# Kernel tuning notes

Hardware: AMD Instinct MI355X
Metric: run time of the kernel (lower is better)

Reference implementation:

```python
import jax, jax.numpy as jnp
import numpy as np

EPS_LN = 1e-5
EPS_COS = 1e-8
EPS_AREA = 5e-4


def _ln(x, g, b):
    m = jnp.mean(x, axis=-1, keepdims=True)
    v = jnp.mean((x - m) ** 2, axis=-1, keepdims=True)
    return (x - m) / jnp.sqrt(v + EPS_LN) * g + b


def _wgap(f, m):
    # f: (b, N, c), m: (b, N) -> (b, c); matches masked avg_pool2d trick
    num = jnp.einsum('bnc,bn->bc', f, m)
    den = jnp.sum(m, axis=1, keepdims=True) + EPS_AREA
    return num / den


def _cos_tok(k, p):
    # k: (b, N, c) tokens vs p: (b, c) prototype, cosine over channel dim
    dot = jnp.einsum('bnc,bc->bn', k, p)
    nk = jnp.linalg.norm(k, axis=-1)
    np_ = jnp.linalg.norm(p, axis=-1, keepdims=True)
    return dot / (jnp.maximum(nk, EPS_COS) * jnp.maximum(np_, EPS_COS))


def _cos_vec(a, b):
    # a, b: (b, c) -> (b,)
    dot = jnp.sum(a * b, axis=-1)
    na = jnp.linalg.norm(a, axis=-1)
    nb = jnp.linalg.norm(b, axis=-1)
    return dot / (jnp.maximum(na, EPS_COS) * jnp.maximum(nb, EPS_COS))


def _mlp(x, W1, b1, W2, b2):
    h = jax.nn.gelu(x @ W1.T + b1, approximate=False)
    return h @ W2.T + b2


def setup_inputs() -> dict:
    key = jax.random.key(0)
    ks = jax.random.split(key, 32)
    b, H, W, c = 8, 64, 64, 512
    N = H * W
    hid = 4 * c
    s = 0.02
    inp = {
        'x': jax.random.normal(ks[0], (b, N, c), jnp.float32),
        'y': jax.random.normal(ks[1], (b, N, c), jnp.float32),
        'mask': (jax.random.uniform(ks[2], (b, N)) > 0.5).astype(jnp.float32),
        'pro_pred': jax.random.uniform(ks[3], (b, 1, H, W), jnp.float32),
        'g1': jnp.ones((c,), jnp.float32), 'beta1': jnp.zeros((c,), jnp.float32),
        'g2': jnp.ones((c,), jnp.float32), 'beta2': jnp.zeros((c,), jnp.float32),
        'Wq': jax.random.normal(ks[4], (c, c)) * s,
        'Wk': jax.random.normal(ks[5], (c, c)) * s,
        'Wv': jax.random.normal(ks[6], (c, c)) * s,
        'Wx1': jax.random.normal(ks[7], (c, 2 * c)) * s,
        'Wx2': jax.random.normal(ks[8], (c, 2 * c)) * s,
        'Wfx': jax.random.normal(ks[9], (c, 2 * c)) * s,
        'Wy1': jax.random.normal(ks[10], (c, 2 * c)) * s,
        'Wy2': jax.random.normal(ks[11], (c, 2 * c)) * s,
        'Wfy': jax.random.normal(ks[12], (c, 2 * c)) * s,
        'W1x': jax.random.normal(ks[13], (hid, c)) * s, 'b1x': jnp.zeros((hid,)),
        'W2x': jax.random.normal(ks[14], (c, hid)) * s, 'b2x': jnp.zeros((c,)),
        'W1y': jax.random.normal(ks[15], (hid, c)) * s, 'b1y': jnp.zeros((hid,)),
        'W2y': jax.random.normal(ks[16], (c, hid)) * s, 'b2y': jnp.zeros((c,)),
        'h': 64, 'w': 64,
    }
    return inp


def reference(x, y, mask, pro_pred, g1, beta1, g2, beta2, Wq, Wk, Wv,
              Wx1, Wx2, Wfx, Wy1, Wy2, Wfy,
              W1x, b1x, W2x, b2x, W1y, b1y, W2y, b2y, h, w):
    b, N, c = x.shape
    x_skip, y_skip = x, y
    xn = _ln(x, g1, beta1)
    yn = _ln(y, g1, beta1)
    q = yn @ Wq.T            # support features (b, N, c)
    k = xn @ Wk.T            # query features
    v = xn @ Wv.T

    m = mask                 # (b, N)
    fg_pro = _wgap(q, m)             # (b, c)
    bg_pro = _wgap(q, 1.0 - m)

    sim_fg = _cos_tok(k, fg_pro) * 10.0   # (b, N)
    sim_bg = _cos_tok(k, bg_pro) * 10.0
    logits = jnp.stack([sim_bg, sim_fg], axis=1)     # (b, 2, N)
    pseudo = jax.nn.softmax(logits, axis=1)

    query_fg1 = _wgap(v, pseudo[:, 1, :])            # (b, c)
    s1 = (_cos_vec(query_fg1, fg_pro)[:, None] + 1.0) / 2.0
    pro1 = s1 * fg_pro + (1.0 - s1) * query_fg1      # (b, c)

    query_fg2 = _wgap(v, pro_pred.reshape(b, N))
    s2 = (_cos_vec(query_fg2, fg_pro)[:, None] + 1.0) / 2.0
    pro2 = s2 * fg_pro + (1.0 - s2) * query_fg2

    p1 = jnp.broadcast_to(pro1[:, None, :], (b, N, c))
    p2 = jnp.broadcast_to(pro2[:, None, :], (b, N, c))

    x1 = jnp.concatenate([x_skip, p1], axis=-1) @ Wx1.T
    x2 = jnp.concatenate([x_skip, p2], axis=-1) @ Wx2.T
    x_merge = jnp.concatenate([x1, x2], axis=-1) @ Wfx.T + x_skip

    y1 = jnp.concatenate([y_skip, p1], axis=-1) @ Wy1.T
    y2 = jnp.concatenate([y_skip, p2], axis=-1) @ Wy2.T
    y_merge = jnp.concatenate([y1, y2], axis=-1) @ Wfy.T + y_skip

    x_out = x + _mlp(_ln(x_merge, g2, beta2), W1x, b1x, W2x, b2x)
    y_out = y + _mlp(_ln(y_merge, g2, beta2), W1y, b1y, W2y, b2y)
    pseudo_mask = pseudo.reshape(b, 2, h, w)
    return x_out, y_out, pseudo_mask
```

## Files before the change

kernel.cpp:

```cpp
#include <hip/hip_runtime.h>
#include <stdint.h>

typedef unsigned short u16;
typedef unsigned int   u32;

typedef __attribute__((ext_vector_type(8))) __bf16 bf16x8;
typedef __attribute__((ext_vector_type(4))) float  f32x4;

#define GLD_LDS(g, l) __builtin_amdgcn_global_load_lds( \
    (__attribute__((address_space(1))) void*)(g),        \
    (__attribute__((address_space(3))) void*)(l), 16, 0, 0)

__device__ __forceinline__ float bf2f(u16 h) {
    union { u32 u; float f; } c; c.u = ((u32)h) << 16; return c.f;
}
__device__ __forceinline__ u16 f2bf(float f) {
    union { float f; u32 u; } c; c.f = f;
    return (u16)((c.u + 0x7FFFu + ((c.u >> 16) & 1u)) >> 16);
}
__device__ __forceinline__ u32 pack2(float a, float b) {
    return (u32)f2bf(a) | ((u32)f2bf(b) << 16);
}
__device__ __forceinline__ uint4 pack8(float4 a, float4 b) {
    return make_uint4(pack2(a.x, a.y), pack2(a.z, a.w), pack2(b.x, b.y), pack2(b.z, b.w));
}
__device__ __forceinline__ void unpack8(uint4 u, float v[8]) {
    v[0] = bf2f((u16)(u.x & 0xffff)); v[1] = bf2f((u16)(u.x >> 16));
    v[2] = bf2f((u16)(u.y & 0xffff)); v[3] = bf2f((u16)(u.y >> 16));
    v[4] = bf2f((u16)(u.z & 0xffff)); v[5] = bf2f((u16)(u.z >> 16));
    v[6] = bf2f((u16)(u.w & 0xffff)); v[7] = bf2f((u16)(u.w >> 16));
}
__device__ __forceinline__ float wsum(float v) {
#pragma unroll
    for (int o = 32; o > 0; o >>= 1) v += __shfl_xor(v, o, 64);
    return v;
}
__device__ __forceinline__ float fast_gelu(float x) {
    const float u = x * (1.f + 0.044715f * x * x);
    return x / (1.f + __expf(-1.5957691216f * u));
}

__global__ __launch_bounds__(256)
void cvt_kernel(const float* __restrict__ in, u16* __restrict__ out, int n8)
{
    const int i = blockIdx.x * 256 + threadIdx.x;
    if (i < n8) {
        const float* p = in + (size_t)i * 8;
        float4 a = *(const float4*)p, b = *(const float4*)(p + 4);
        *(uint4*)(out + (size_t)i * 8) = pack8(a, b);
    }
}

template<bool IN16, bool RAW>
__global__ __launch_bounds__(256)
void ln_kernel(const void* __restrict__ in, u16* __restrict__ out,
               const float* __restrict__ g, const float* __restrict__ be,
               u16* __restrict__ raw_out)
{
    const int lane = threadIdx.x & 63;
    const size_t row = (size_t)blockIdx.x * 4 + (threadIdx.x >> 6);
    const size_t base = row * 512 + lane * 8;
    float v[8];
    if constexpr (IN16) {
        unpack8(*(const uint4*)((const u16*)in + base), v);
    } else {
        const float* p = (const float*)in + base;
        float4 a = *(const float4*)p, b = *(const float4*)(p + 4);
        v[0]=a.x; v[1]=a.y; v[2]=a.z; v[3]=a.w; v[4]=b.x; v[5]=b.y; v[6]=b.z; v[7]=b.w;
    }
    if constexpr (RAW) {
        u32 ro[4];
#pragma unroll
        for (int i = 0; i < 4; ++i) ro[i] = pack2(v[2*i], v[2*i+1]);
        *(uint4*)(raw_out + base) = make_uint4(ro[0], ro[1], ro[2], ro[3]);
    }
    float s = 0.f, ss = 0.f;
#pragma unroll
    for (int i = 0; i < 8; ++i) { s += v[i]; ss += v[i] * v[i]; }
    s = wsum(s); ss = wsum(ss);
    const float mean = s * (1.f / 512.f);
    const float rstd = rsqrtf(ss * (1.f / 512.f) - mean * mean + 1e-5f);
    const float* gp = g + lane * 8;
    const float* bp = be + lane * 8;
    u32 o[4];
#pragma unroll
    for (int i = 0; i < 4; ++i) {
        u16 lo = f2bf((v[2*i]   - mean) * rstd * gp[2*i]   + bp[2*i]);
        u16 hi = f2bf((v[2*i+1] - mean) * rstd * gp[2*i+1] + bp[2*i+1]);
        o[i] = (u32)lo | ((u32)hi << 16);
    }
    *(uint4*)(out + base) = make_uint4(o[0], o[1], o[2], o[3]);
}

template<bool IS16>
__device__ __forceinline__ void load_pair(const void* P, size_t off, size_t rstep,
                                          uint4& r0, uint4& r1)
{
    if constexpr (IS16) {
        const u16* p = (const u16*)P + off;
        r0 = *(const uint4*)p;
        r1 = *(const uint4*)(p + rstep);
    } else {
        const float* p = (const float*)P + off;
        float4 a0 = *(const float4*)p,           a1 = *(const float4*)(p + 4);
        float4 b0 = *(const float4*)(p + rstep), b1 = *(const float4*)(p + rstep + 4);
        r0 = pack8(a0, a1);
        r1 = pack8(b0, b1);
    }
}

template<int EPI, bool OUT16>
__global__ __launch_bounds__(512)
void gemm3_kernel(const u16* __restrict__ A, const u16* __restrict__ B,
                  void* __restrict__ Cp, int N, int K,
                  const float* __restrict__ bias_b,
                  const float* __restrict__ bias_v,
                  const float* __restrict__ skip)
{
    __shared__ u16 sA[2][128 * 32];
    __shared__ u16 sB[2][256 * 32];
    const int t = threadIdx.x;
    const int w = t >> 6;
    const int lane = t & 63;
    const int lr = lane & 15;
    const int lk = lane >> 4;
    const int bm0 = blockIdx.x * 128;
    const int bn0 = blockIdx.y * 256;
    const int wrow = (w >> 2) * 64;
    const int wcol = (w & 3) * 64;

    f32x4 acc[4][4];
#pragma unroll
    for (int m = 0; m < 4; ++m)
#pragma unroll
        for (int n = 0; n < 4; ++n) acc[m][n] = (f32x4){0.f, 0.f, 0.f, 0.f};

    const int scol = ((t & 3) ^ ((t >> 3) & 3)) * 8;
    const u16* gA = A + (size_t)(bm0 + (t >> 2)) * K + scol;
    const u16* gB = B + (size_t)(bn0 + (t >> 2)) * K + scol;
    const size_t rstep = (size_t)128 * K;
    const int wo = w << 9;
    const int sa = (lk ^ ((lr >> 1) & 3)) * 8;

    GLD_LDS(gA, sA[0] + wo);
    GLD_LDS(gB, sB[0] + wo);
    GLD_LDS(gB + rstep, sB[0] + 4096 + wo);
    __syncthreads();

    int cur = 0;
    for (int kt = 32; kt <= K; kt += 32) {
        if (kt < K) {
            const int nxt = cur ^ 1;
            GLD_LDS(gA + kt, sA[nxt] + wo);
            GLD_LDS(gB + kt, sB[nxt] + wo);
            GLD_LDS(gB + kt + rstep, sB[nxt] + 4096 + wo);
        }
        bf16x8 af[4], bfr[4];
#pragma unroll
        for (int m = 0; m < 4; ++m)
            af[m] = *(const bf16x8*)&sA[cur][(wrow + m * 16 + lr) * 32 + sa];
#pragma unroll
        for (int n = 0; n < 4; ++n)
            bfr[n] = *(const bf16x8*)&sB[cur][(wcol + n * 16 + lr) * 32 + sa];
#pragma unroll
        for (int m = 0; m < 4; ++m)
#pragma unroll
            for (int n = 0; n < 4; ++n)
                acc[m][n] = __builtin_amdgcn_mfma_f32_16x16x32_bf16(af[m], bfr[n], acc[m][n], 0, 0, 0);
        if (kt < K) { __syncthreads(); cur ^= 1; }
    }

#pragma unroll
    for (int m = 0; m < 4; ++m) {
#pragma unroll
        for (int n = 0; n < 4; ++n) {
            const int col = bn0 + wcol + n * 16 + lr;
#pragma unroll
            for (int r = 0; r < 4; ++r) {
                const int row = bm0 + wrow + m * 16 + lk * 4 + r;
                const size_t idx = (size_t)row * N + col;
                float vv = acc[m][n][r];
                if (EPI == 1) vv += bias_b[(size_t)(row >> 12) * N + col] + skip[idx];
                if (EPI == 2) { vv += bias_v[col]; vv = fast_gelu(vv); }
                if (EPI == 3) vv += bias_v[col] + skip[idx];
                if (OUT16) ((u16*)Cp)[idx] = f2bf(vv);
                else       ((float*)Cp)[idx] = vv;
            }
        }
    }
}

template<int EPI, bool OUT16>
__global__ __launch_bounds__(256)
void gemm2_kernel(const u16* __restrict__ A, const u16* __restrict__ B,
                  void* __restrict__ Cp, int N, int K,
                  const float* __restrict__ bias_b,
                  const float* __restrict__ bias_v,
                  const float* __restrict__ skip)
{
    __shared__ u16 sA[2][128 * 32];
    __shared__ u16 sB[2][128 * 32];
    const int t = threadIdx.x;
    const int w = t >> 6;
    const int lane = t & 63;
    const int lr = lane & 15;
    const int lk = lane >> 4;
    const int bm0 = blockIdx.x * 128;
    const int bn0 = blockIdx.y * 128;
    const int wrow = (w >> 1) * 64;
    const int wcol = (w & 1) * 64;

    f32x4 acc[4][4];
#pragma unroll
    for (int m = 0; m < 4; ++m)
#pragma unroll
        for (int n = 0; n < 4; ++n) acc[m][n] = (f32x4){0.f, 0.f, 0.f, 0.f};

    const int scol = ((t & 3) ^ ((t >> 3) & 3)) * 8;
    const u16* gA = A + (size_t)(bm0 + (t >> 2)) * K + scol;
    const u16* gB = B + (size_t)(bn0 + (t >> 2)) * K + scol;
    const size_t rstep = (size_t)64 * K;
    const int wo = w << 9;
    const int sa = (lk ^ ((lr >> 1) & 3)) * 8;

    GLD_LDS(gA, sA[0] + wo); GLD_LDS(gA + rstep, sA[0] + wo + 2048);
    GLD_LDS(gB, sB[0] + wo); GLD_LDS(gB + rstep, sB[0] + wo + 2048);
    __syncthreads();

    int cur = 0;
    for (int kt = 32; kt <= K; kt += 32) {
        if (kt < K) {
            const int nxt = cur ^ 1;
            GLD_LDS(gA + kt, sA[nxt] + wo); GLD_LDS(gA + kt + rstep, sA[nxt] + wo + 2048);
            GLD_LDS(gB + kt, sB[nxt] + wo); GLD_LDS(gB + kt + rstep, sB[nxt] + wo + 2048);
        }
        bf16x8 af[4], bfr[4];
#pragma unroll
        for (int m = 0; m < 4; ++m)
            af[m] = *(const bf16x8*)&sA[cur][(wrow + m * 16 + lr) * 32 + sa];
#pragma unroll
        for (int n = 0; n < 4; ++n)
            bfr[n] = *(const bf16x8*)&sB[cur][(wcol + n * 16 + lr) * 32 + sa];
#pragma unroll
        for (int m = 0; m < 4; ++m)
#pragma unroll
            for (int n = 0; n < 4; ++n)
                acc[m][n] = __builtin_amdgcn_mfma_f32_16x16x32_bf16(af[m], bfr[n], acc[m][n], 0, 0, 0);
        if (kt < K) { __syncthreads(); cur ^= 1; }
    }

#pragma unroll
    for (int m = 0; m < 4; ++m) {
#pragma unroll
        for (int n = 0; n < 4; ++n) {
            const int col = bn0 + wcol + n * 16 + lr;
#pragma unroll
            for (int r = 0; r < 4; ++r) {
                const int row = bm0 + wrow + m * 16 + lk * 4 + r;
                const size_t idx = (size_t)row * N + col;
                float vv = acc[m][n][r];
                if (EPI == 1) vv += bias_b[(size_t)(row >> 12) * N + col] + skip[idx];
                if (EPI == 2) { vv += bias_v[col]; vv = fast_gelu(vv); }
                if (EPI == 3) vv += bias_v[col] + skip[idx];
                if (OUT16) ((u16*)Cp)[idx] = f2bf(vv);
                else       ((float*)Cp)[idx] = vv;
            }
        }
    }
}

template<int WM>
__global__ __launch_bounds__(512)
void gemm3_red_kernel(const u16* __restrict__ A, const u16* __restrict__ B, int K,
                      const float* __restrict__ wa, const float* __restrict__ wb,
                      float* __restrict__ acc1, float* __restrict__ acc2)
{
    __shared__ u16 sA[2][128 * 32];
    __shared__ u16 sB[2][256 * 32];
    __shared__ float sred[8][2][64];
    const int t = threadIdx.x;
    const int w = t >> 6;
    const int lane = t & 63;
    const int lr = lane & 15;
    const int lk = lane >> 4;
    const int bm0 = blockIdx.x * 128;
    const int bn0 = blockIdx.y * 256;
    const int wrow = (w >> 2) * 64;
    const int wcol = (w & 3) * 64;

    f32x4 acc[4][4];
#pragma unroll
    for (int m = 0; m < 4; ++m)
#pragma unroll
        for (int n = 0; n < 4; ++n) acc[m][n] = (f32x4){0.f, 0.f, 0.f, 0.f};

    const int scol = ((t & 3) ^ ((t >> 3) & 3)) * 8;
    const u16* gA = A + (size_t)(bm0 + (t >> 2)) * K + scol;
    const u16* gB = B + (size_t)(bn0 + (t >> 2)) * K + scol;
    const size_t rstep = (size_t)128 * K;
    const int wo = w << 9;
    const int sa = (lk ^ ((lr >> 1) & 3)) * 8;

    GLD_LDS(gA, sA[0] + wo);
    GLD_LDS(gB, sB[0] + wo);
    GLD_LDS(gB + rstep, sB[0] + 4096 + wo);
    __syncthreads();

    int cur = 0;
    for (int kt = 32; kt <= K; kt += 32) {
        if (kt < K) {
            const int nxt = cur ^ 1;
            GLD_LDS(gA + kt, sA[nxt] + wo);
            GLD_LDS(gB + kt, sB[nxt] + wo);
            GLD_LDS(gB + kt + rstep, sB[nxt] + 4096 + wo);
        }
        bf16x8 af[4], bfr[4];
#pragma unroll
        for (int m = 0; m < 4; ++m)
            af[m] = *(const bf16x8*)&sA[cur][(wrow + m * 16 + lr) * 32 + sa];
#pragma unroll
        for (int n = 0; n < 4; ++n)
            bfr[n] = *(const bf16x8*)&sB[cur][(wcol + n * 16 + lr) * 32 + sa];
#pragma unroll
        for (int m = 0; m < 4; ++m)
#pragma unroll
            for (int n = 0; n < 4; ++n)
                acc[m][n] = __builtin_amdgcn_mfma_f32_16x16x32_bf16(af[m], bfr[n], acc[m][n], 0, 0, 0);
        if (kt < K) { __syncthreads(); cur ^= 1; }
    }

    float w1v[16], w2v[16];
#pragma unroll
    for (int m = 0; m < 4; ++m)
#pragma unroll
        for (int r = 0; r < 4; ++r) {
            const int row = bm0 + wrow + m * 16 + lk * 4 + r;
            if (WM == 0) { float mm = wa[row]; w1v[m*4+r] = mm; w2v[m*4+r] = 1.f - mm; }
            else         { w1v[m*4+r] = wa[row]; w2v[m*4+r] = wb[row]; }
        }
    __syncthreads();
#pragma unroll
    for (int n = 0; n < 4; ++n) {
        float s1 = 0.f, s2 = 0.f;
#pragma unroll
        for (int m = 0; m < 4; ++m)
#pragma unroll
            for (int r = 0; r < 4; ++r) {
                s1 += acc[m][n][r] * w1v[m*4+r];
                s2 += acc[m][n][r] * w2v[m*4+r];
            }
        s1 += __shfl_xor(s1, 16, 64); s1 += __shfl_xor(s1, 32, 64);
        s2 += __shfl_xor(s2, 16, 64); s2 += __shfl_xor(s2, 32, 64);
        if (lk == 0) { sred[w][0][n*16+lr] = s1; sred[w][1][n*16+lr] = s2; }
    }
    __syncthreads();
    if (t < 256) {
        const int strip = t >> 6, c = t & 63;
        const float v1 = sred[strip][0][c] + sred[strip + 4][0][c];
        const float v2 = sred[strip][1][c] + sred[strip + 4][1][c];
        const int col = bn0 + strip * 64 + c;
        const int b = bm0 >> 12;
        atomicAdd(&acc1[b * 512 + col], v1);
        atomicAdd(&acc2[b * 512 + col], v2);
    }
}

template<int EPI, bool A16, bool B16, bool OUT16>
__global__ __launch_bounds__(256)
void gemm_kernel(const void* __restrict__ Ap, const void* __restrict__ Wp,
                 void* __restrict__ Cp, int N, int K,
                 const float* __restrict__ bias_b,
                 const float* __restrict__ bias_v,
                 const float* __restrict__ skip)
{
    __shared__ u16 sA[128 * 32];
    __shared__ u16 sB[128 * 32];
    const int t = threadIdx.x;
    const int w = t >> 6;
    const int lane = t & 63;
    const int lr = lane & 15;
    const int lk = lane >> 4;
    const int bm0 = blockIdx.x * 128;
    const int bn0 = blockIdx.y * 128;
    const int wrow = (w >> 1) * 64;
    const int wcol = (w & 1) * 64;

    f32x4 acc[4][4];
#pragma unroll
    for (int m = 0; m < 4; ++m)
#pragma unroll
        for (int n = 0; n < 4; ++n) acc[m][n] = (f32x4){0.f, 0.f, 0.f, 0.f};

    const size_t aoff = (size_t)(bm0 + (t >> 2)) * K + (t & 3) * 8;
    const size_t boff = (size_t)(bn0 + (t >> 2)) * K + (t & 3) * 8;
    const size_t rstep = (size_t)64 * K;
    u16* dA = sA + 8 * t;
    u16* dB = sB + 8 * t;

    for (int kt = 0; kt < K; kt += 32) {
        uint4 ra0, ra1, rb0, rb1;
        load_pair<A16>(Ap, aoff + kt, rstep, ra0, ra1);
        load_pair<B16>(Wp, boff + kt, rstep, rb0, rb1);
        __syncthreads();
        *(uint4*)dA = ra0; *(uint4*)(dA + 2048) = ra1;
        *(uint4*)dB = rb0; *(uint4*)(dB + 2048) = rb1;
        __syncthreads();
        bf16x8 af[4], bfr[4];
#pragma unroll
        for (int m = 0; m < 4; ++m)
            af[m] = *(const bf16x8*)&sA[(wrow + m * 16 + lr) * 32 + lk * 8];
#pragma unroll
        for (int n = 0; n < 4; ++n)
            bfr[n] = *(const bf16x8*)&sB[(wcol + n * 16 + lr) * 32 + lk * 8];
#pragma unroll
        for (int m = 0; m < 4; ++m)
#pragma unroll
            for (int n = 0; n < 4; ++n)
                acc[m][n] = __builtin_amdgcn_mfma_f32_16x16x32_bf16(af[m], bfr[n], acc[m][n], 0, 0, 0);
    }

#pragma unroll
    for (int m = 0; m < 4; ++m) {
#pragma unroll
        for (int n = 0; n < 4; ++n) {
            const int col = bn0 + wcol + n * 16 + lr;
#pragma unroll
            for (int r = 0; r < 4; ++r) {
                const int row = bm0 + wrow + m * 16 + lk * 4 + r;
                const size_t idx = (size_t)row * N + col;
                float vv = acc[m][n][r];
                if (EPI == 1) vv += bias_b[(size_t)(row >> 12) * N + col] + skip[idx];
                if (EPI == 2) { vv += bias_v[col]; vv = fast_gelu(vv); }
                if (EPI == 3) vv += bias_v[col] + skip[idx];
                if (OUT16) ((u16*)Cp)[idx] = f2bf(vv);
                else       ((float*)Cp)[idx] = vv;
            }
        }
    }
}

template<int WM>
__global__ __launch_bounds__(256)
void gemm_red_kernel(const u16* __restrict__ A, const float* __restrict__ W, int K,
                     const float* __restrict__ wa, const float* __restrict__ wb,
                     float* __restrict__ acc1, float* __restrict__ acc2)
{
    __shared__ u16 sA[128 * 32];
    __shared__ u16 sB[128 * 32];
    __shared__ float sred[4][2][64];
    const int t = threadIdx.x;
    const int w = t >> 6;
    const int lane = t & 63;
    const int lr = lane & 15;
    const int lk = lane >> 4;
    const int bm0 = blockIdx.x * 128;
    const int bn0 = blockIdx.y * 128;
    const int wrow = (w >> 1) * 64;
    const int wcol = (w & 1) * 64;

    f32x4 acc[4][4];
#pragma unroll
    for (int m = 0; m < 4; ++m)
#pragma unroll
        for (int n = 0; n < 4; ++n) acc[m][n] = (f32x4){0.f, 0.f, 0.f, 0.f};

    const size_t aoff = (size_t)(bm0 + (t >> 2)) * K + (t & 3) * 8;
    const size_t boff = (size_t)(bn0 + (t >> 2)) * K + (t & 3) * 8;
    const size_t rstep = (size_t)64 * K;
    u16* dA = sA + 8 * t;
    u16* dB = sB + 8 * t;

    for (int kt = 0; kt < K; kt += 32) {
        uint4 ra0, ra1, rb0, rb1;
        load_pair<true >(A, aoff + kt, rstep, ra0, ra1);
        load_pair<false>(W, boff + kt, rstep, rb0, rb1);
        __syncthreads();
        *(uint4*)dA = ra0; *(uint4*)(dA + 2048) = ra1;
        *(uint4*)dB = rb0; *(uint4*)(dB + 2048) = rb1;
        __syncthreads();
        bf16x8 af[4], bfr[4];
#pragma unroll
        for (int m = 0; m < 4; ++m)
            af[m] = *(const bf16x8*)&sA[(wrow + m * 16 + lr) * 32 + lk * 8];
#pragma unroll
        for (int n = 0; n < 4; ++n)
            bfr[n] = *(const bf16x8*)&sB[(wcol + n * 16 + lr) * 32 + lk * 8];
#pragma unroll
        for (int m = 0; m < 4; ++m)
#pragma unroll
            for (int n = 0; n < 4; ++n)
                acc[m][n] = __builtin_amdgcn_mfma_f32_16x16x32_bf16(af[m], bfr[n], acc[m][n], 0, 0, 0);
    }

    float w1v[16], w2v[16];
#pragma unroll
    for (int m = 0; m < 4; ++m)
#pragma unroll
        for (int r = 0; r < 4; ++r) {
            const int row = bm0 + wrow + m * 16 + lk * 4 + r;
            if (WM == 0) { float mm = wa[row]; w1v[m*4+r] = mm; w2v[m*4+r] = 1.f - mm; }
            else         { w1v[m*4+r] = wa[row]; w2v[m*4+r] = wb[row]; }
        }
#pragma unroll
    for (int n = 0; n < 4; ++n) {
        float s1 = 0.f, s2 = 0.f;
#pragma unroll
        for (int m = 0; m < 4; ++m)
#pragma unroll
            for (int r = 0; r < 4; ++r) {
                s1 += acc[m][n][r] * w1v[m*4+r];
                s2 += acc[m][n][r] * w2v[m*4+r];
            }
        s1 += __shfl_xor(s1, 16, 64); s1 += __shfl_xor(s1, 32, 64);
        s2 += __shfl_xor(s2, 16, 64); s2 += __shfl_xor(s2, 32, 64);
        if (lk == 0) { sred[w][0][n*16+lr] = s1; sred[w][1][n*16+lr] = s2; }
    }
    __syncthreads();
    if (t < 128) {
        const int half = t >> 6, c = t & 63;
        const float v1 = sred[half][0][c] + sred[half + 2][0][c];
        const float v2 = sred[half][1][c] + sred[half + 2][1][c];
        const int col = bn0 + half * 64 + c;
        const int b = bm0 >> 12;
        atomicAdd(&acc1[b * 512 + col], v1);
        atomicAdd(&acc2[b * 512 + col], v2);
    }
}

__global__ __launch_bounds__(256)
void rowsum_kernel(const float* __restrict__ in, float* __restrict__ out)
{
    __shared__ float sred[4];
    const int b = blockIdx.x, t = threadIdx.x;
    float s = 0.f;
    for (int i = 0; i < 16; ++i) s += in[b * 4096 + t + i * 256];
    s = wsum(s);
    if ((t & 63) == 0) sred[t >> 6] = s;
    __syncthreads();
    if (t == 0) out[b] = sred[0] + sred[1] + sred[2] + sred[3];
}

__global__ __launch_bounds__(512)
void proto_fin_kernel(const float* __restrict__ fgacc, const float* __restrict__ bgacc,
                      const float* __restrict__ denfg, float* __restrict__ fg_pro,
                      float* __restrict__ bg_pro, float* __restrict__ nfg, float* __restrict__ nbg)
{
    __shared__ float sred[16];
    const int b = blockIdx.x, c = threadIdx.x;
    const float d = denfg[b];
    const float fg = fgacc[b * 512 + c] / (d + 5e-4f);
    const float bg = bgacc[b * 512 + c] / ((4096.f - d) + 5e-4f);
    fg_pro[b * 512 + c] = fg; bg_pro[b * 512 + c] = bg;
    float s1 = wsum(fg * fg), s2 = wsum(bg * bg);
    if ((c & 63) == 0) { sred[c >> 6] = s1; sred[8 + (c >> 6)] = s2; }
    __syncthreads();
    if (c == 0) {
        float a = 0.f, bb = 0.f;
        for (int i = 0; i < 8; ++i) { a += sred[i]; bb += sred[8 + i]; }
        nfg[b] = sqrtf(a); nbg[b] = sqrtf(bb);
    }
}

__global__ __launch_bounds__(256)
void sim_kernel(const u16* __restrict__ k, const float* __restrict__ fg_pro,
                const float* __restrict__ bg_pro, const float* __restrict__ nfg,
                const float* __restrict__ nbg, float* __restrict__ pseudo_fg,
                float* __restrict__ pm)
{
    const int lane = threadIdx.x & 63;
    const int token = blockIdx.x * 4 + (threadIdx.x >> 6);
    const int b = token >> 12, n = token & 4095;
    uint4 u = *(const uint4*)(k + (size_t)token * 512 + lane * 8);
    float kv[8]; unpack8(u, kv);
    const float* fp = fg_pro + b * 512 + lane * 8;
    const float* bp = bg_pro + b * 512 + lane * 8;
    float dfg = 0.f, dbg = 0.f, kk = 0.f;
#pragma unroll
    for (int i = 0; i < 8; ++i) { dfg += kv[i] * fp[i]; dbg += kv[i] * bp[i]; kk += kv[i] * kv[i]; }
    dfg = wsum(dfg); dbg = wsum(dbg); kk = wsum(kk);
    const float nk = fmaxf(sqrtf(kk), 1e-8f);
    const float sfg = 10.f * dfg / (nk * fmaxf(nfg[b], 1e-8f));
    const float sbg = 10.f * dbg / (nk * fmaxf(nbg[b], 1e-8f));
    const float pfg = 1.f / (1.f + expf(sbg - sfg));
    if (lane == 0) {
        pseudo_fg[token] = pfg;
        pm[(size_t)b * 8192 + 4096 + n] = pfg;
        pm[(size_t)b * 8192 + n] = 1.f - pfg;
    }
}

__global__ __launch_bounds__(512)
void proto2_kernel(const float* __restrict__ q1acc, const float* __restrict__ q2acc,
                   const float* __restrict__ denq1, const float* __restrict__ denq2,
                   const float* __restrict__ fg_pro, const float* __restrict__ nfg,
                   float* __restrict__ pro1, float* __restrict__ pro2)
{
    __shared__ float sred[32];
    __shared__ float s1s, s2s;
    const int b = blockIdx.x, c = threadIdx.x;
    const float q1 = q1acc[b * 512 + c] / (denq1[b] + 5e-4f);
    const float q2 = q2acc[b * 512 + c] / (denq2[b] + 5e-4f);
    const float fg = fg_pro[b * 512 + c];
    float r0 = wsum(q1 * fg), r1 = wsum(q1 * q1), r2 = wsum(q2 * fg), r3 = wsum(q2 * q2);
    const int wv = c >> 6;
    if ((c & 63) == 0) { sred[wv] = r0; sred[8 + wv] = r1; sred[16 + wv] = r2; sred[24 + wv] = r3; }
    __syncthreads();
    if (c == 0) {
        float d1 = 0.f, n1 = 0.f, d2 = 0.f, n2 = 0.f;
        for (int i = 0; i < 8; ++i) { d1 += sred[i]; n1 += sred[8+i]; d2 += sred[16+i]; n2 += sred[24+i]; }
        const float nf = fmaxf(nfg[b], 1e-8f);
        s1s = (d1 / (fmaxf(sqrtf(n1), 1e-8f) * nf) + 1.f) * 0.5f;
        s2s = (d2 / (fmaxf(sqrtf(n2), 1e-8f) * nf) + 1.f) * 0.5f;
    }
    __syncthreads();
    pro1[b * 512 + c] = s1s * fg + (1.f - s1s) * q1;
    pro2[b * 512 + c] = s2s * fg + (1.f - s2s) * q2;
}

__global__ __launch_bounds__(256)
void mmcomb_kernel(const float* __restrict__ Wf, const float* __restrict__ W1,
                   const float* __restrict__ W2, u16* __restrict__ Mout)
{
    const int i = blockIdx.x * 16 + threadIdx.x;
    const int o = blockIdx.y * 16 + threadIdx.y;
    float s = 0.f;
    for (int j = 0; j < 512; ++j) {
        s += Wf[o * 1024 + j]       * W1[j * 1024 + i];
        s += Wf[o * 1024 + 512 + j] * W2[j * 1024 + i];
    }
    Mout[o * 512 + i] = f2bf(s);
}

__global__ __launch_bounds__(512)
void tvec_kernel(const float* __restrict__ W, const float* __restrict__ p, float* __restrict__ tout)
{
    const int lane = threadIdx.x & 63;
    const int j = blockIdx.x * 8 + (threadIdx.x >> 6);
    const int b = blockIdx.y;
    const float* wr = W + (size_t)j * 1024 + 512 + lane * 8;
    const float* pr = p + b * 512 + lane * 8;
    float4 w0 = *(const float4*)wr, w1 = *(const float4*)(wr + 4);
    float4 p0 = *(const float4*)pr, p1 = *(const float4*)(pr + 4);
    float s = w0.x*p0.x + w0.y*p0.y + w0.z*p0.z + w0.w*p0.w
            + w1.x*p1.x + w1.y*p1.y + w1.z*p1.z + w1.w*p1.w;
    s = wsum(s);
    if (lane == 0) tout[b * 512 + j] = s;
}

__global__ __launch_bounds__(512)
void biascomb_kernel(const float* __restrict__ Wf, const float* __restrict__ t1,
                     const float* __restrict__ t2, float* __restrict__ bias)
{
    const int lane = threadIdx.x & 63;
    const int o = blockIdx.x * 8 + (threadIdx.x >> 6);
    const int b = blockIdx.y;
    const float* w1 = Wf + (size_t)o * 1024 + lane * 8;
    const float* tp1 = t1 + b * 512 + lane * 8;
    const float* tp2 = t2 + b * 512 + lane * 8;
    float s = 0.f;
#pragma unroll
    for (int h = 0; h < 2; ++h) {
        const float* wv = w1 + h * 512;
        const float* tp = h ? tp2 : tp1;
        float4 a0 = *(const float4*)wv, a1 = *(const float4*)(wv + 4);
        float4 b0 = *(const float4*)tp, b1 = *(const float4*)(tp + 4);
        s += a0.x*b0.x + a0.y*b0.y + a0.z*b0.z + a0.w*b0.w
           + a1.x*b1.x + a1.y*b1.y + a1.z*b1.z + a1.w*b1.w;
    }
    s = wsum(s);
    if (lane == 0) bias[b * 512 + o] = s;
}

extern "C" void kernel_launch(void* const* d_in, const int* in_sizes, int n_in,
                              void* d_out, int out_size, void* d_ws, size_t ws_size,
                              hipStream_t stream)
{
    const float* x   = (const float*)d_in[0];
    const float* y   = (const float*)d_in[1];
    const float* mask= (const float*)d_in[2];
    const float* pp  = (const float*)d_in[3];
    const float* g1  = (const float*)d_in[4];
    const float* be1 = (const float*)d_in[5];
    const float* g2  = (const float*)d_in[6];
    const float* be2 = (const float*)d_in[7];
    const float* Wq  = (const float*)d_in[8];
    const float* Wk  = (const float*)d_in[9];
    const float* Wv  = (const float*)d_in[10];
    const float* Wx1 = (const float*)d_in[11];
    const float* Wx2 = (const float*)d_in[12];
    const float* Wfx = (const float*)d_in[13];
    const float* Wy1 = (const float*)d_in[14];
    const float* Wy2 = (const float*)d_in[15];
    const float* Wfy = (const float*)d_in[16];
    const float* W1x = (const float*)d_in[17];
    const float* b1x = (const float*)d_in[18];
    const float* W2x = (const float*)d_in[19];
    const float* b2x = (const float*)d_in[20];
    const float* W1y = (const float*)d_in[21];
    const float* b1y = (const float*)d_in[22];
    const float* W2y = (const float*)d_in[23];
    const float* b2y = (const float*)d_in[24];

    if (ws_size < 69206016u) return;
    const bool fast = ws_size >= 78643200u;
    const bool huge = ws_size >= 145752064u;

    float* outx = (float*)d_out;
    float* outy = outx + 16777216;
    float* pmf  = outx + 33554432;

    char* wsb = (char*)d_ws;
    float* fsm = (float*)wsb;
    float* fgacc  = fsm;
    float* bgacc  = fsm + 4096;
    float* q1acc  = fsm + 8192;
    float* q2acc  = fsm + 12288;
    float* denq1  = fsm + 16384;
    float* denfg  = fsm + 16392;
    float* denq2  = fsm + 16400;
    float* nfg    = fsm + 16408;
    float* nbg    = fsm + 16416;
    float* fg_pro = fsm + 16424;
    float* bg_pro = fsm + 20520;
    float* pro1   = fsm + 24616;
    float* pro2   = fsm + 28712;
    float* t1x    = fsm + 32808;
    float* t2x    = fsm + 36904;
    float* t1y    = fsm + 41000;
    float* t2y    = fsm + 45096;
    float* bias_x = fsm + 49192;
    float* bias_y = fsm + 53288;
    float* pseudo = fsm + 57384;

    hipMemsetAsync(fsm, 0, 65568, stream);

    if (fast) {
        u16* Mx   = (u16*)(wsb + 0x60000);
        u16* My   = (u16*)(wsb + 0xE0000);
        u16* Wqb  = (u16*)(wsb + 0x160000);
        u16* Wkb  = (u16*)(wsb + 0x1E0000);
        u16* Wvb  = (u16*)(wsb + 0x260000);
        u16* W1xb = (u16*)(wsb + 0x2E0000);
        u16* W2xb = (u16*)(wsb + 0x4E0000);
        u16* W1yb = (u16*)(wsb + 0x6E0000);
        u16* W2yb = (u16*)(wsb + 0x8E0000);
        u16* WS0  = (u16*)(wsb + 0xB00000);
        u16* WS1  = WS0 + 16777216;
        u16* WS2  = WS1 + 16777216;

        u16* OX0 = (u16*)outx;
        u16* OX1 = OX0 + 16777216;
        u16* OY  = (u16*)outy;

        cvt_kernel<<<128, 256, 0, stream>>>(Wq,  Wqb,  32768);
        cvt_kernel<<<128, 256, 0, stream>>>(Wk,  Wkb,  32768);
        cvt_kernel<<<128, 256, 0, stream>>>(Wv,  Wvb,  32768);
        cvt_kernel<<<512, 256, 0, stream>>>(W1x, W1xb, 131072);
        cvt_kernel<<<512, 256, 0, stream>>>(W2x, W2xb, 131072);
        cvt_kernel<<<512, 256, 0, stream>>>(W1y, W1yb, 131072);
        cvt_kernel<<<512, 256, 0, stream>>>(W2y, W2yb, 131072);
        mmcomb_kernel<<<dim3(32, 32), dim3(16, 16), 0, stream>>>(Wfx, Wx1, Wx2, Mx);
        mmcomb_kernel<<<dim3(32, 32), dim3(16, 16), 0, stream>>>(Wfy, Wy1, Wy2, My);

        ln_kernel<false, true><<<8192, 256, 0, stream>>>(x, WS0, g1, be1, OX0);
        ln_kernel<false, true><<<8192, 256, 0, stream>>>(y, WS1, g1, be1, OY);

        dim3 gq(256, 2);
        gemm3_red_kernel<0><<<gq, 512, 0, stream>>>(WS1, Wqb, 512, mask, nullptr, fgacc, bgacc);
        rowsum_kernel<<<8, 256, 0, stream>>>(mask, denfg);
        rowsum_kernel<<<8, 256, 0, stream>>>(pp, denq2);
        proto_fin_kernel<<<8, 512, 0, stream>>>(fgacc, bgacc, denfg, fg_pro, bg_pro, nfg, nbg);

        gemm3_kernel<0, true><<<gq, 512, 0, stream>>>(WS0, Wkb, OX1, 512, 512, nullptr, nullptr, nullptr);
        sim_kernel<<<8192, 256, 0, stream>>>(OX1, fg_pro, bg_pro, nfg, nbg, pseudo, pmf);
        rowsum_kernel<<<8, 256, 0, stream>>>(pseudo, denq1);

        gemm3_red_kernel<1><<<gq, 512, 0, stream>>>(WS0, Wvb, 512, pseudo, pp, q1acc, q2acc);
        proto2_kernel<<<8, 512, 0, stream>>>(q1acc, q2acc, denq1, denq2, fg_pro, nfg, pro1, pro2);

        dim3 gtv(64, 8);
        tvec_kernel<<<gtv, 512, 0, stream>>>(Wx1, pro1, t1x);
        tvec_kernel<<<gtv, 512, 0, stream>>>(Wx2, pro2, t2x);
        tvec_kernel<<<gtv, 512, 0, stream>>>(Wy1, pro1, t1y);
        tvec_kernel<<<gtv, 512, 0, stream>>>(Wy2, pro2, t2y);
        biascomb_kernel<<<gtv, 512, 0, stream>>>(Wfx, t1x, t2x, bias_x);
        biascomb_kernel<<<gtv, 512, 0, stream>>>(Wfy, t1y, t2y, bias_y);

        gemm3_kernel<1, true><<<gq, 512, 0, stream>>>(OX0, Mx, WS0, 512, 512, bias_x, nullptr, x);
        ln_kernel<true, false><<<8192, 256, 0, stream>>>(WS0, WS1, g2, be2, nullptr);
        gemm3_kernel<1, true><<<gq, 512, 0, stream>>>(OY, My, WS0, 512, 512, bias_y, nullptr, y);
        ln_kernel<true, false><<<8192, 256, 0, stream>>>(WS0, WS0, g2, be2, nullptr);

        for (int ch = 0; ch < 2; ++ch) {
            const size_t ro = (size_t)ch * 16384 * 512;
            gemm3_kernel<2, true><<<dim3(128, 8), 512, 0, stream>>>(WS1 + ro, W1xb, OY, 2048, 512, nullptr, b1x, nullptr);
            gemm2_kernel<3, false><<<dim3(128, 4), 256, 0, stream>>>(OY, W2xb, outx + ro, 512, 2048, nullptr, b2x, x + ro);
        }

        if (huge) {
            for (int ch = 0; ch < 2; ++ch) {
                const size_t ro = (size_t)ch * 16384 * 512;
                gemm3_kernel<2, true><<<dim3(128, 8), 512, 0, stream>>>(WS0 + ro, W1yb, WS2, 2048, 512, nullptr, b1y, nullptr);
                gemm2_kernel<3, false><<<dim3(128, 4), 256, 0, stream>>>(WS2, W2yb, outy + ro, 512, 2048, nullptr, b2y, y + ro);
            }
        } else {
            for (int ch = 0; ch < 4; ++ch) {
                const size_t ro = (size_t)ch * 8192 * 512;
                gemm3_kernel<2, true><<<dim3(64, 8), 512, 0, stream>>>(WS0 + ro, W1yb, WS1, 2048, 512, nullptr, b1y, nullptr);
                gemm2_kernel<3, false><<<dim3(64, 4), 256, 0, stream>>>(WS1, W2yb, outy + ro, 512, 2048, nullptr, b2y, y + ro);
            }
        }
    } else {
        u16* Mx  = (u16*)(wsb + 360608);
        u16* My  = (u16*)(wsb + 884896);
        u16* WS0 = (u16*)(wsb + 2097152);
        u16* WS1 = (u16*)(wsb + 35651584);

        ln_kernel<false, false><<<8192, 256, 0, stream>>>(x, WS0, g1, be1, nullptr);
        ln_kernel<false, false><<<8192, 256, 0, stream>>>(y, WS1, g1, be1, nullptr);

        dim3 g512(256, 4);
        gemm_red_kernel<0><<<g512, 256, 0, stream>>>(WS1, Wq, 512, mask, nullptr, fgacc, bgacc);
        rowsum_kernel<<<8, 256, 0, stream>>>(mask, denfg);
        rowsum_kernel<<<8, 256, 0, stream>>>(pp, denq2);
        proto_fin_kernel<<<8, 512, 0, stream>>>(fgacc, bgacc, denfg, fg_pro, bg_pro, nfg, nbg);

        gemm_kernel<0, true, false, true><<<g512, 256, 0, stream>>>(WS0, Wk, WS1, 512, 512, nullptr, nullptr, nullptr);
        sim_kernel<<<8192, 256, 0, stream>>>(WS1, fg_pro, bg_pro, nfg, nbg, pseudo, pmf);
        rowsum_kernel<<<8, 256, 0, stream>>>(pseudo, denq1);

        gemm_red_kernel<1><<<g512, 256, 0, stream>>>(WS0, Wv, 512, pseudo, pp, q1acc, q2acc);
        proto2_kernel<<<8, 512, 0, stream>>>(q1acc, q2acc, denq1, denq2, fg_pro, nfg, pro1, pro2);

        mmcomb_kernel<<<dim3(32, 32), dim3(16, 16), 0, stream>>>(Wfx, Wx1, Wx2, Mx);
        mmcomb_kernel<<<dim3(32, 32), dim3(16, 16), 0, stream>>>(Wfy, Wy1, Wy2, My);
        dim3 gtv(64, 8);
        tvec_kernel<<<gtv, 512, 0, stream>>>(Wx1, pro1, t1x);
        tvec_kernel<<<gtv, 512, 0, stream>>>(Wx2, pro2, t2x);
        tvec_kernel<<<gtv, 512, 0, stream>>>(Wy1, pro1, t1y);
        tvec_kernel<<<gtv, 512, 0, stream>>>(Wy2, pro2, t2y);
        biascomb_kernel<<<gtv, 512, 0, stream>>>(Wfx, t1x, t2x, bias_x);
        biascomb_kernel<<<gtv, 512, 0, stream>>>(Wfy, t1y, t2y, bias_y);

        gemm_kernel<1, false, true, true><<<g512, 256, 0, stream>>>(x, Mx, WS0, 512, 512, bias_x, nullptr, x);
        ln_kernel<true, false><<<8192, 256, 0, stream>>>(WS0, WS1, g2, be2, nullptr);
        for (int ch = 0; ch < 4; ++ch) {
            const size_t ro = (size_t)ch * 8192 * 512;
            gemm_kernel<2, true, false, true><<<dim3(64, 16), 256, 0, stream>>>(WS1 + ro, W1x, WS0, 2048, 512, nullptr, b1x, nullptr);
            gemm_kernel<3, true, false, false><<<dim3(64, 4), 256, 0, stream>>>(WS0, W2x, outx + ro, 512, 2048, nullptr, b2x, x + ro);
        }
        gemm_kernel<1, false, true, true><<<g512, 256, 0, stream>>>(y, My, WS0, 512, 512, bias_y, nullptr, y);
        ln_kernel<true, false><<<8192, 256, 0, stream>>>(WS0, WS1, g2, be2, nullptr);
        for (int ch = 0; ch < 4; ++ch) {
            const size_t ro = (size_t)ch * 8192 * 512;
            gemm_kernel<2, true, false, true><<<dim3(64, 16), 256, 0, stream>>>(WS1 + ro, W1y, WS0, 2048, 512, nullptr, b1y, nullptr);
            gemm_kernel<3, true, false, false><<<dim3(64, 4), 256, 0, stream>>>(WS0, W2y, outy + ro, 512, 2048, nullptr, b2y, y + ro);
        }
    }
    (void)in_sizes; (void)n_in; (void)out_size;
}
```

Baseline: 903.6 us.

## Enlarge GEMM block tile to 256x256 with K-step 64

```diff
diff --git a/kernel.cpp b/kernel.cpp
--- a/kernel.cpp
+++ b/kernel.cpp
@@ -111,73 +111,82 @@
 
 template<int EPI, bool OUT16>
 __global__ __launch_bounds__(512)
-void gemm3_kernel(const u16* __restrict__ A, const u16* __restrict__ B,
+void gemm5_kernel(const u16* __restrict__ A, const u16* __restrict__ B,
                   void* __restrict__ Cp, int N, int K,
                   const float* __restrict__ bias_b,
                   const float* __restrict__ bias_v,
                   const float* __restrict__ skip)
 {
-    __shared__ u16 sA[2][128 * 32];
-    __shared__ u16 sB[2][256 * 32];
+    __shared__ u16 sA[2][256 * 64];
+    __shared__ u16 sB[2][256 * 64];
     const int t = threadIdx.x;
     const int w = t >> 6;
     const int lane = t & 63;
     const int lr = lane & 15;
     const int lk = lane >> 4;
-    const int bm0 = blockIdx.x * 128;
+    const int bm0 = blockIdx.x * 256;
     const int bn0 = blockIdx.y * 256;
-    const int wrow = (w >> 2) * 64;
-    const int wcol = (w & 3) * 64;
-
-    f32x4 acc[4][4];
-#pragma unroll
-    for (int m = 0; m < 4; ++m)
+    const int wr = (w >> 2) * 128;
+    const int wc = (w & 3) * 64;
+
+    f32x4 acc[8][4];
+#pragma unroll
+    for (int m = 0; m < 8; ++m)
 #pragma unroll
         for (int n = 0; n < 4; ++n) acc[m][n] = (f32x4){0.f, 0.f, 0.f, 0.f};
 
-    const int scol = ((t & 3) ^ ((t >> 3) & 3)) * 8;
-    const u16* gA = A + (size_t)(bm0 + (t >> 2)) * K + scol;
-    const u16* gB = B + (size_t)(bn0 + (t >> 2)) * K + scol;
-    const size_t rstep = (size_t)128 * K;
-    const int wo = w << 9;
-    const int sa = (lk ^ ((lr >> 1) & 3)) * 8;
-
-    GLD_LDS(gA, sA[0] + wo);
-    GLD_LDS(gB, sB[0] + wo);
-    GLD_LDS(gB + rstep, sB[0] + 4096 + wo);
+    const int srow = w * 8 + (lane >> 3);
+    const int schunk = ((lane & 7) ^ (lane >> 3)) * 8;
+    const u16* gA = A + (size_t)(bm0 + srow) * K + schunk;
+    const u16* gB = B + (size_t)(bn0 + srow) * K + schunk;
+    const size_t rstep64 = (size_t)64 * K;
+    const int ldso = w * 512;
+    const int cbase = (lk ^ (lr & 7)) * 8;
+
+#pragma unroll
+    for (int i = 0; i < 4; ++i) {
+        GLD_LDS(gA + i * rstep64, sA[0] + i * 4096 + ldso);
+        GLD_LDS(gB + i * rstep64, sB[0] + i * 4096 + ldso);
+    }
     __syncthreads();
 
     int cur = 0;
-    for (int kt = 32; kt <= K; kt += 32) {
+    for (int kt = 64; kt <= K; kt += 64) {
         if (kt < K) {
             const int nxt = cur ^ 1;
-            GLD_LDS(gA + kt, sA[nxt] + wo);
-            GLD_LDS(gB + kt, sB[nxt] + wo);
-            GLD_LDS(gB + kt + rstep, sB[nxt] + 4096 + wo);
-        }
-        bf16x8 af[4], bfr[4];
-#pragma unroll
-        for (int m = 0; m < 4; ++m)
-            af[m] = *(const bf16x8*)&sA[cur][(wrow + m * 16 + lr) * 32 + sa];
-#pragma unroll
-        for (int n = 0; n < 4; ++n)
-            bfr[n] = *(const bf16x8*)&sB[cur][(wcol + n * 16 + lr) * 32 + sa];
-#pragma unroll
-        for (int m = 0; m < 4; ++m)
+#pragma unroll
+            for (int i = 0; i < 4; ++i) {
+                GLD_LDS(gA + kt + i * rstep64, sA[nxt] + i * 4096 + ldso);
+                GLD_LDS(gB + kt + i * rstep64, sB[nxt] + i * 4096 + ldso);
+            }
+        }
+#pragma unroll
+        for (int kk = 0; kk < 2; ++kk) {
+            const int co = cbase ^ (kk << 5);
+            bf16x8 af[8], bfr[4];
+#pragma unroll
+            for (int m = 0; m < 8; ++m)
+                af[m] = *(const bf16x8*)&sA[cur][(wr + m * 16 + lr) * 64 + co];
 #pragma unroll
             for (int n = 0; n < 4; ++n)
-                acc[m][n] = __builtin_amdgcn_mfma_f32_16x16x32_bf16(af[m], bfr[n], acc[m][n], 0, 0, 0);
+                bfr[n] = *(const bf16x8*)&sB[cur][(wc + n * 16 + lr) * 64 + co];
+#pragma unroll
+            for (int m = 0; m < 8; ++m)
+#pragma unroll
+                for (int n = 0; n < 4; ++n)
+                    acc[m][n] = __builtin_amdgcn_mfma_f32_16x16x32_bf16(af[m], bfr[n], acc[m][n], 0, 0, 0);
+        }
         if (kt < K) { __syncthreads(); cur ^= 1; }
     }
 
 #pragma unroll
-    for (int m = 0; m < 4; ++m) {
+    for (int m = 0; m < 8; ++m) {
 #pragma unroll
         for (int n = 0; n < 4; ++n) {
-            const int col = bn0 + wcol + n * 16 + lr;
+            const int col = bn0 + wc + n * 16 + lr;
 #pragma unroll
             for (int r = 0; r < 4; ++r) {
-                const int row = bm0 + wrow + m * 16 + lk * 4 + r;
+                const int row = bm0 + wr + m * 16 + lk * 4 + r;
                 const size_t idx = (size_t)row * N + col;
                 float vv = acc[m][n][r];
                 if (EPI == 1) vv += bias_b[(size_t)(row >> 12) * N + col] + skip[idx];
@@ -771,7 +780,8 @@
         rowsum_kernel<<<8, 256, 0, stream>>>(pp, denq2);
         proto_fin_kernel<<<8, 512, 0, stream>>>(fgacc, bgacc, denfg, fg_pro, bg_pro, nfg, nbg);
 
-        gemm3_kernel<0, true><<<gq, 512, 0, stream>>>(WS0, Wkb, OX1, 512, 512, nullptr, nullptr, nullptr);
+        dim3 g5q(128, 2);
+        gemm5_kernel<0, true><<<g5q, 512, 0, stream>>>(WS0, Wkb, OX1, 512, 512, nullptr, nullptr, nullptr);
         sim_kernel<<<8192, 256, 0, stream>>>(OX1, fg_pro, bg_pro, nfg, nbg, pseudo, pmf);
         rowsum_kernel<<<8, 256, 0, stream>>>(pseudo, denq1);
 
@@ -786,27 +796,27 @@
         biascomb_kernel<<<gtv, 512, 0, stream>>>(Wfx, t1x, t2x, bias_x);
         biascomb_kernel<<<gtv, 512, 0, stream>>>(Wfy, t1y, t2y, bias_y);
 
-        gemm3_kernel<1, true><<<gq, 512, 0, stream>>>(OX0, Mx, WS0, 512, 512, bias_x, nullptr, x);
+        gemm5_kernel<1, true><<<g5q, 512, 0, stream>>>(OX0, Mx, WS0, 512, 512, bias_x, nullptr, x);
         ln_kernel<true, false><<<8192, 256, 0, stream>>>(WS0, WS1, g2, be2, nullptr);
-        gemm3_kernel<1, true><<<gq, 512, 0, stream>>>(OY, My, WS0, 512, 512, bias_y, nullptr, y);
+        gemm5_kernel<1, true><<<g5q, 512, 0, stream>>>(OY, My, WS0, 512, 512, bias_y, nullptr, y);
         ln_kernel<true, false><<<8192, 256, 0, stream>>>(WS0, WS0, g2, be2, nullptr);
 
         for (int ch = 0; ch < 2; ++ch) {
             const size_t ro = (size_t)ch * 16384 * 512;
-            gemm3_kernel<2, true><<<dim3(128, 8), 512, 0, stream>>>(WS1 + ro, W1xb, OY, 2048, 512, nullptr, b1x, nullptr);
+            gemm5_kernel<2, true><<<dim3(64, 8), 512, 0, stream>>>(WS1 + ro, W1xb, OY, 2048, 512, nullptr, b1x, nullptr);
             gemm2_kernel<3, false><<<dim3(128, 4), 256, 0, stream>>>(OY, W2xb, outx + ro, 512, 2048, nullptr, b2x, x + ro);
         }
 
         if (huge) {
             for (int ch = 0; ch < 2; ++ch) {
                 const size_t ro = (size_t)ch * 16384 * 512;
-                gemm3_kernel<2, true><<<dim3(128, 8), 512, 0, stream>>>(WS0 + ro, W1yb, WS2, 2048, 512, nullptr, b1y, nullptr);
+                gemm5_kernel<2, true><<<dim3(64, 8), 512, 0, stream>>>(WS0 + ro, W1yb, WS2, 2048, 512, nullptr, b1y, nullptr);
                 gemm2_kernel<3, false><<<dim3(128, 4), 256, 0, stream>>>(WS2, W2yb, outy + ro, 512, 2048, nullptr, b2y, y + ro);
             }
         } else {
             for (int ch = 0; ch < 4; ++ch) {
                 const size_t ro = (size_t)ch * 8192 * 512;
-                gemm3_kernel<2, true><<<dim3(64, 8), 512, 0, stream>>>(WS0 + ro, W1yb, WS1, 2048, 512, nullptr, b1y, nullptr);
+                gemm5_kernel<2, true><<<dim3(32, 8), 512, 0, stream>>>(WS0 + ro, W1yb, WS1, 2048, 512, nullptr, b1y, nullptr);
                 gemm2_kernel<3, false><<<dim3(64, 4), 256, 0, stream>>>(WS1, W2yb, outy + ro, 512, 2048, nullptr, b2y, y + ro);
             }
         }
```

After: 933.4 us. 3.3% more time.

## Swizzle GEMM block order and batch small conversion/tvec launches

Applied to the files above, without the earlier changes.

```diff
diff --git a/kernel.cpp b/kernel.cpp
--- a/kernel.cpp
+++ b/kernel.cpp
@@ -39,16 +39,42 @@
     const float u = x * (1.f + 0.044715f * x * x);
     return x / (1.f + __expf(-1.5957691216f * u));
 }
+__device__ __forceinline__ void swz_block(int& bx, int& by) {
+    const int gx = gridDim.x;
+    const int n = gx * gridDim.y;
+    int f = blockIdx.y * gx + blockIdx.x;
+    f = (f & 7) * (n >> 3) + (f >> 3);
+    bx = f % gx; by = f / gx;
+}
 
 __global__ __launch_bounds__(256)
-void cvt_kernel(const float* __restrict__ in, u16* __restrict__ out, int n8)
+void cvt4_kernel(const float* __restrict__ a, const float* __restrict__ b,
+                 const float* __restrict__ c, const float* __restrict__ d,
+                 u16* __restrict__ oa, u16* __restrict__ ob,
+                 u16* __restrict__ oc, u16* __restrict__ od, int n8)
 {
     const int i = blockIdx.x * 256 + threadIdx.x;
-    if (i < n8) {
-        const float* p = in + (size_t)i * 8;
-        float4 a = *(const float4*)p, b = *(const float4*)(p + 4);
-        *(uint4*)(out + (size_t)i * 8) = pack8(a, b);
-    }
+    if (i >= n8) return;
+    const int z = blockIdx.y;
+    const float* in = (z == 0) ? a : (z == 1) ? b : (z == 2) ? c : d;
+    u16* out = (z == 0) ? oa : (z == 1) ? ob : (z == 2) ? oc : od;
+    const float* p = in + (size_t)i * 8;
+    float4 u = *(const float4*)p, v = *(const float4*)(p + 4);
+    *(uint4*)(out + (size_t)i * 8) = pack8(u, v);
+}
+__global__ __launch_bounds__(256)
+void cvt3_kernel(const float* __restrict__ a, const float* __restrict__ b,
+                 const float* __restrict__ c,
+                 u16* __restrict__ oa, u16* __restrict__ ob, u16* __restrict__ oc, int n8)
+{
+    const int i = blockIdx.x * 256 + threadIdx.x;
+    if (i >= n8) return;
+    const int z = blockIdx.y;
+    const float* in = (z == 0) ? a : (z == 1) ? b : c;
+    u16* out = (z == 0) ? oa : (z == 1) ? ob : oc;
+    const float* p = in + (size_t)i * 8;
+    float4 u = *(const float4*)p, v = *(const float4*)(p + 4);
+    *(uint4*)(out + (size_t)i * 8) = pack8(u, v);
 }
 
 template<bool IN16, bool RAW>
@@ -119,13 +145,14 @@
 {
     __shared__ u16 sA[2][128 * 32];
     __shared__ u16 sB[2][256 * 32];
+    int bxi, byi; swz_block(bxi, byi);
     const int t = threadIdx.x;
     const int w = t >> 6;
     const int lane = t & 63;
     const int lr = lane & 15;
     const int lk = lane >> 4;
-    const int bm0 = blockIdx.x * 128;
-    const int bn0 = blockIdx.y * 256;
+    const int bm0 = bxi * 128;
+    const int bn0 = byi * 256;
     const int wrow = (w >> 2) * 64;
     const int wcol = (w & 3) * 64;
 
@@ -200,13 +227,14 @@
 {
     __shared__ u16 sA[2][128 * 32];
     __shared__ u16 sB[2][128 * 32];
+    int bxi, byi; swz_block(bxi, byi);
     const int t = threadIdx.x;
     const int w = t >> 6;
     const int lane = t & 63;
     const int lr = lane & 15;
     const int lk = lane >> 4;
-    const int bm0 = blockIdx.x * 128;
-    const int bn0 = blockIdx.y * 128;
+    const int bm0 = bxi * 128;
+    const int bn0 = byi * 128;
     const int wrow = (w >> 1) * 64;
     const int wcol = (w & 1) * 64;
 
@@ -278,13 +306,14 @@
     __shared__ u16 sA[2][128 * 32];
     __shared__ u16 sB[2][256 * 32];
     __shared__ float sred[8][2][64];
+    int bxi, byi; swz_block(bxi, byi);
     const int t = threadIdx.x;
     const int w = t >> 6;
     const int lane = t & 63;
     const int lr = lane & 15;
     const int lk = lane >> 4;
-    const int bm0 = blockIdx.x * 128;
-    const int bn0 = blockIdx.y * 256;
+    const int bm0 = bxi * 128;
+    const int bn0 = byi * 256;
     const int wrow = (w >> 2) * 64;
     const int wcol = (w & 3) * 64;
 
@@ -632,8 +661,16 @@
 }
 
 __global__ __launch_bounds__(512)
-void tvec_kernel(const float* __restrict__ W, const float* __restrict__ p, float* __restrict__ tout)
-{
+void tvec4_kernel(const float* __restrict__ Wx1, const float* __restrict__ Wx2,
+                  const float* __restrict__ Wy1, const float* __restrict__ Wy2,
+                  const float* __restrict__ pro1, const float* __restrict__ pro2,
+                  float* __restrict__ t1x, float* __restrict__ t2x,
+                  float* __restrict__ t1y, float* __restrict__ t2y)
+{
+    const int z = blockIdx.z;
+    const float* W = (z == 0) ? Wx1 : (z == 1) ? Wx2 : (z == 2) ? Wy1 : Wy2;
+    const float* p = (z & 1) ? pro2 : pro1;
+    float* tout = (z == 0) ? t1x : (z == 1) ? t2x : (z == 2) ? t1y : t2y;
     const int lane = threadIdx.x & 63;
     const int j = blockIdx.x * 8 + (threadIdx.x >> 6);
     const int b = blockIdx.y;
@@ -648,9 +685,16 @@
 }
 
 __global__ __launch_bounds__(512)
-void biascomb_kernel(const float* __restrict__ Wf, const float* __restrict__ t1,
-                     const float* __restrict__ t2, float* __restrict__ bias)
-{
+void biascomb2_kernel(const float* __restrict__ Wfx, const float* __restrict__ Wfy,
+                      const float* __restrict__ t1x, const float* __restrict__ t2x,
+                      const float* __restrict__ t1y, const float* __restrict__ t2y,
+                      float* __restrict__ bias_x, float* __restrict__ bias_y)
+{
+    const int z = blockIdx.z;
+    const float* Wf = z ? Wfy : Wfx;
+    const float* t1 = z ? t1y : t1x;
+    const float* t2 = z ? t2y : t2x;
+    float* bias = z ? bias_y : bias_x;
     const int lane = threadIdx.x & 63;
     const int o = blockIdx.x * 8 + (threadIdx.x >> 6);
     const int b = blockIdx.y;
@@ -752,13 +796,8 @@
         u16* OX1 = OX0 + 16777216;
         u16* OY  = (u16*)outy;
 
-        cvt_kernel<<<128, 256, 0, stream>>>(Wq,  Wqb,  32768);
-        cvt_kernel<<<128, 256, 0, stream>>>(Wk,  Wkb,  32768);
-        cvt_kernel<<<128, 256, 0, stream>>>(Wv,  Wvb,  32768);
-        cvt_kernel<<<512, 256, 0, stream>>>(W1x, W1xb, 131072);
-        cvt_kernel<<<512, 256, 0, stream>>>(W2x, W2xb, 131072);
-        cvt_kernel<<<512, 256, 0, stream>>>(W1y, W1yb, 131072);
-        cvt_kernel<<<512, 256, 0, stream>>>(W2y, W2yb, 131072);
+        cvt3_kernel<<<dim3(128, 3), 256, 0, stream>>>(Wq, Wk, Wv, Wqb, Wkb, Wvb, 32768);
+        cvt4_kernel<<<dim3(512, 4), 256, 0, stream>>>(W1x, W2x, W1y, W2y, W1xb, W2xb, W1yb, W2yb, 131072);
         mmcomb_kernel<<<dim3(32, 32), dim3(16, 16), 0, stream>>>(Wfx, Wx1, Wx2, Mx);
         mmcomb_kernel<<<dim3(32, 32), dim3(16, 16), 0, stream>>>(Wfy, Wy1, Wy2, My);
 
@@ -778,13 +817,8 @@
         gemm3_red_kernel<1><<<gq, 512, 0, stream>>>(WS0, Wvb, 512, pseudo, pp, q1acc, q2acc);
         proto2_kernel<<<8, 512, 0, stream>>>(q1acc, q2acc, denq1, denq2, fg_pro, nfg, pro1, pro2);
 
-        dim3 gtv(64, 8);
-        tvec_kernel<<<gtv, 512, 0, stream>>>(Wx1, pro1, t1x);
-        tvec_kernel<<<gtv, 512, 0, stream>>>(Wx2, pro2, t2x);
-        tvec_kernel<<<gtv, 512, 0, stream>>>(Wy1, pro1, t1y);
-        tvec_kernel<<<gtv, 512, 0, stream>>>(Wy2, pro2, t2y);
-        biascomb_kernel<<<gtv, 512, 0, stream>>>(Wfx, t1x, t2x, bias_x);
-        biascomb_kernel<<<gtv, 512, 0, stream>>>(Wfy, t1y, t2y, bias_y);
+        tvec4_kernel<<<dim3(64, 8, 4), 512, 0, stream>>>(Wx1, Wx2, Wy1, Wy2, pro1, pro2, t1x, t2x, t1y, t2y);
+        biascomb2_kernel<<<dim3(64, 8, 2), 512, 0, stream>>>(Wfx, Wfy, t1x, t2x, t1y, t2y, bias_x, bias_y);
 
         gemm3_kernel<1, true><<<gq, 512, 0, stream>>>(OX0, Mx, WS0, 512, 512, bias_x, nullptr, x);
         ln_kernel<true, false><<<8192, 256, 0, stream>>>(WS0, WS1, g2, be2, nullptr);
@@ -834,13 +868,8 @@
 
         mmcomb_kernel<<<dim3(32, 32), dim3(16, 16), 0, stream>>>(Wfx, Wx1, Wx2, Mx);
         mmcomb_kernel<<<dim3(32, 32), dim3(16, 16), 0, stream>>>(Wfy, Wy1, Wy2, My);
-        dim3 gtv(64, 8);
-        tvec_kernel<<<gtv, 512, 0, stream>>>(Wx1, pro1, t1x);
-        tvec_kernel<<<gtv, 512, 0, stream>>>(Wx2, pro2, t2x);
-        tvec_kernel<<<gtv, 512, 0, stream>>>(Wy1, pro1, t1y);
-        tvec_kernel<<<gtv, 512, 0, stream>>>(Wy2, pro2, t2y);
-        biascomb_kernel<<<gtv, 512, 0, stream>>>(Wfx, t1x, t2x, bias_x);
-        biascomb_kernel<<<gtv, 512, 0, stream>>>(Wfy, t1y, t2y, bias_y);
+        tvec4_kernel<<<dim3(64, 8, 4), 512, 0, stream>>>(Wx1, Wx2, Wy1, Wy2, pro1, pro2, t1x, t2x, t1y, t2y);
+        biascomb2_kernel<<<dim3(64, 8, 2), 512, 0, stream>>>(Wfx, Wfy, t1x, t2x, t1y, t2y, bias_x, bias_y);
 
         gemm_kernel<1, false, true, true><<<g512, 256, 0, stream>>>(x, Mx, WS0, 512, 512, bias_x, nullptr, x);
         ln_kernel<true, false><<<8192, 256, 0, stream>>>(WS0, WS1, g2, be2, nullptr);
```

Result: no change. 897.8 us (-0.6%).
